# Performance work log

Hardware: AMD Instinct MI355X
Metric: run time of the kernel (lower is better)

## Reference

```python
import jax, jax.numpy as jnp
import numpy as np

TEX = 256  # texture grid resolution hardcoded in the module


def _grid_sample_bilinear(img, grid):
    """torch.F.grid_sample(img, grid): bilinear, zero padding, align_corners=False.
    img: [B,C,H,W]; grid: [B,Hg,Wg,2] in [-1,1] (x,y order). Returns [B,C,Hg,Wg]."""
    B, C, H, W = img.shape
    gx = (grid[..., 0] + 1.0) * (W * 0.5) - 0.5  # pixel-space x
    gy = (grid[..., 1] + 1.0) * (H * 0.5) - 0.5  # pixel-space y
    x0 = jnp.floor(gx)
    y0 = jnp.floor(gy)
    wx1 = gx - x0
    wy1 = gy - y0

    def corner(xi, yi, w):
        valid = (xi >= 0) & (xi <= W - 1) & (yi >= 0) & (yi <= H - 1)
        xc = jnp.clip(xi, 0, W - 1).astype(jnp.int32)
        yc = jnp.clip(yi, 0, H - 1).astype(jnp.int32)
        # per-batch gather: [B,C,Hg,Wg]
        v = jax.vmap(lambda im, yy, xx: im[:, yy, xx])(img, yc, xc)
        return v * (w * valid.astype(img.dtype))[:, None, :, :]

    return (corner(x0, y0, (1 - wx1) * (1 - wy1))
            + corner(x0 + 1, y0, wx1 * (1 - wy1))
            + corner(x0, y0 + 1, (1 - wx1) * wy1)
            + corner(x0 + 1, y0 + 1, wx1 * wy1))


def setup_inputs() -> dict:
    key = jax.random.key(0)
    k1, k2, k3, k4, k5, k6 = jax.random.split(key, 6)
    B, V, P, HW = 16, 5023, 60000, 512
    source_img = jax.random.uniform(k1, (B, 3, HW, HW), dtype=jnp.float32)
    target_mesh_v = jax.random.normal(k2, (B, V, 3), dtype=jnp.float32) * 0.1
    vertex_normals = jax.random.normal(k3, (B, V, 3), dtype=jnp.float32)
    # camera: [scale, tx, ty]; scale near 8-10 typical for DECA crops, keep ~1 range here
    camera_params = jnp.concatenate([
        jax.random.uniform(k4, (B, 1), minval=5.0, maxval=10.0),
        jax.random.uniform(k4, (B, 2), minval=-0.05, maxval=0.05)], axis=1).astype(jnp.float32)
    valid_pixel_3d_faces = jax.random.randint(k5, (P, 3), 0, V, dtype=jnp.int32)
    bc = jax.random.uniform(k6, (P, 3), dtype=jnp.float32) + 1e-3
    valid_pixel_b_coords = bc / jnp.sum(bc, axis=1, keepdims=True)  # barycentric
    lin = jnp.arange(P, dtype=jnp.int32)  # collision-free texel enumeration
    x_coords = lin % TEX
    y_coords = lin // TEX
    return {"source_img": source_img, "target_mesh_v": target_mesh_v,
            "vertex_normals": vertex_normals, "camera_params": camera_params,
            "valid_pixel_3d_faces": valid_pixel_3d_faces,
            "valid_pixel_b_coords": valid_pixel_b_coords,
            "x_coords": x_coords, "y_coords": y_coords}


def reference(source_img, target_mesh_v, vertex_normals, camera_params,
              valid_pixel_3d_faces, valid_pixel_b_coords, x_coords, y_coords):
    B = source_img.shape[0]
    # gather face vertices and barycentric-interpolate: [B,P,3(verts),3(xyz)] -> [B,P,3]
    tv = target_mesh_v[:, valid_pixel_3d_faces, :]
    pixel_3d_points = jnp.einsum('bpkc,pk->bpc', tv, valid_pixel_b_coords)
    # batch_orth_proj: scale * (xy + txy); then flip y
    cam = camera_params[:, None, :]  # [B,1,3]
    proj_xy = cam[..., 0:1] * (pixel_3d_points[..., :2] + cam[..., 1:3])
    proj_xy = jnp.stack([proj_xy[..., 0], -proj_xy[..., 1]], axis=-1)  # [B,P,2]
    # scatter into 256x256 sampling grid (zeros elsewhere)
    texture_grid = jnp.zeros((B, TEX, TEX, 2), dtype=jnp.float32)
    texture_grid = texture_grid.at[:, y_coords, x_coords, :].set(proj_xy)
    texture_img = _grid_sample_bilinear(source_img, texture_grid)  # [B,3,256,256]
    # interpolated normal z-component for visibility
    nvz = vertex_normals[..., 2][:, valid_pixel_3d_faces]  # [B,P,3]
    pixel_nz = jnp.einsum('bpk,pk->bp', nvz, valid_pixel_b_coords)
    texture_vis_mask = jnp.zeros((B, 1, TEX, TEX), dtype=jnp.bool_)
    texture_vis_mask = texture_vis_mask.at[:, 0, y_coords, x_coords].set(pixel_nz < 0)
    return texture_img, texture_vis_mask
```

## Files before the change

### kernel.cpp

```cpp
#include <hip/hip_runtime.h>
#include <math.h>

#define TEXD 256
#define NT (TEXD * TEXD)
#define BB 16
#define NPAIR (BB / 2)

struct alignas(4) F3 { float x, y, z; };
struct alignas(4) I3 { int a, b, c; };


__global__ void flame_prep_kernel(const float* __restrict__ tmv,
                                  const float* __restrict__ vn,
                                  float4* __restrict__ pv, int V,
                                  const float* __restrict__ img,
                                  uchar4* __restrict__ img8,
                                  int HW, int packBlocks) {
    int bid = blockIdx.x;
    if (bid < packBlocks) {
        int i = bid * 256 + threadIdx.x;
        if (i < BB * V) {
            int b = i / V;
            int v = i - b * V;
            pv[(size_t)v * BB + b] =
                make_float4(tmv[(size_t)i * 3 + 0], tmv[(size_t)i * 3 + 1],
                            vn[(size_t)i * 3 + 2], 0.0f);
        }
    } else {
        int plane = HW * HW;
        int cb = bid - packBlocks;
        int pb = plane / 256;
        int b = cb / pb;
        int off = (cb - b * pb) * 256 + threadIdx.x;
        const float* base = img + (size_t)b * 3 * plane;
        float r = base[off];
        float g = base[off + plane];
        float bl = base[off + 2 * plane];
        img8[(size_t)b * plane + off] =
            make_uchar4((unsigned char)__float2int_rn(r * 255.0f),
                        (unsigned char)__float2int_rn(g * 255.0f),
                        (unsigned char)__float2int_rn(bl * 255.0f), 0);
    }
}

__global__ void flame_project_kernel(const float4* __restrict__ pv,
                                     const float* __restrict__ cam,
                                     const I3* __restrict__ faces,
                                     const F3* __restrict__ bcw,
                                     float4* __restrict__ gridpair,
                                     float* __restrict__ out_mask,
                                     int P) {
    int gid = blockIdx.x * 256 + threadIdx.x;
    int t = gid >> 2;
    int q = gid & 3;

    int bs0 = 2 * q;
    int bs1 = 2 * q + 1;

    float gx[4], gy[4], mk[4];
    if (t < P) {
        I3 f3 = faces[t];
        F3 w3 = bcw[t];
        const float4* ra = pv + (size_t)f3.a * BB;
        const float4* rb = pv + (size_t)f3.b * BB;
        const float4* rc = pv + (size_t)f3.c * BB;
#pragma unroll
        for (int j = 0; j < 4; ++j) {
            int b = (j & 1) ? bs1 : bs0;
            if (j >= 2) b += NPAIR;
            float4 A = ra[b];
            float4 Bv = rb[b];
            float4 C = rc[b];
            float px = A.x * w3.x + Bv.x * w3.y + C.x * w3.z;
            float py = A.y * w3.x + Bv.y * w3.y + C.y * w3.z;
            float nz = A.z * w3.x + Bv.z * w3.y + C.z * w3.z;
            float fo = cam[b * 3 + 0];
            float cx = cam[b * 3 + 1];
            float cy = cam[b * 3 + 2];
            gx[j] = fo * (px + cx);
            gy[j] = -(fo * (py + cy));
            mk[j] = (nz < 0.0f) ? 1.0f : 0.0f;
        }
    } else {
#pragma unroll
        for (int j = 0; j < 4; ++j) { gx[j] = 0.0f; gy[j] = 0.0f; mk[j] = 0.0f; }
    }

    gridpair[(size_t)bs0 * NT + t] = make_float4(gx[0], gy[0], gx[2], gy[2]);
    gridpair[(size_t)bs1 * NT + t] = make_float4(gx[1], gy[1], gx[3], gy[3]);
    out_mask[(size_t)bs0 * NT + t] = mk[0];
    out_mask[(size_t)bs1 * NT + t] = mk[1];
    out_mask[(size_t)(bs0 + NPAIR) * NT + t] = mk[2];
    out_mask[(size_t)(bs1 + NPAIR) * NT + t] = mk[3];
}

__device__ __forceinline__ void sample3_u8(const uchar4* __restrict__ base,
                                           int HW, float gxn, float gyn,
                                           float out[3]) {
    float half = 0.5f * (float)HW;
    float gx = (gxn + 1.0f) * half - 0.5f;
    float gy = (gyn + 1.0f) * half - 0.5f;

    float x0f = floorf(gx);
    float y0f = floorf(gy);
    float wx = gx - x0f;
    float wy = gy - y0f;
    int x0 = (int)x0f;
    int y0 = (int)y0f;
    int x1 = x0 + 1;
    int y1 = y0 + 1;

    bool vx0 = (x0 >= 0) && (x0 <= HW - 1);
    bool vx1 = (x1 >= 0) && (x1 <= HW - 1);
    bool vy0 = (y0 >= 0) && (y0 <= HW - 1);
    bool vy1 = (y1 >= 0) && (y1 <= HW - 1);

    const float s = 1.0f / 255.0f;
    float w00 = (1.0f - wx) * (1.0f - wy) * ((vx0 && vy0) ? s : 0.0f);
    float w01 = wx * (1.0f - wy) * ((vx1 && vy0) ? s : 0.0f);
    float w10 = (1.0f - wx) * wy * ((vx0 && vy1) ? s : 0.0f);
    float w11 = wx * wy * ((vx1 && vy1) ? s : 0.0f);

    int xb = min(max(x0, 0), HW - 2);
    bool lo = (x0 == xb);
    float wl0 = lo ? w00 : w01;
    float wh0 = lo ? w01 : w00;
    float wl1 = lo ? w10 : w11;
    float wh1 = lo ? w11 : w10;

    int cy0 = min(max(y0, 0), HW - 1);
    int cy1 = min(max(y1, 0), HW - 1);
    const uchar4* r0 = base + (size_t)cy0 * HW + xb;
    const uchar4* r1 = base + (size_t)cy1 * HW + xb;
    uchar4 a0 = r0[0], a1 = r0[1];
    uchar4 d0 = r1[0], d1 = r1[1];

    out[0] = a0.x * wl0 + a1.x * wh0 + d0.x * wl1 + d1.x * wh1;
    out[1] = a0.y * wl0 + a1.y * wh0 + d0.y * wl1 + d1.y * wh1;
    out[2] = a0.z * wl0 + a1.z * wh0 + d0.z * wl1 + d1.z * wh1;
}

__global__ void flame_gather_kernel(const uchar4* __restrict__ img8,
                                    const float4* __restrict__ gridpair,
                                    float* __restrict__ out_img,
                                    int HW) {
    int pair = blockIdx.x % NPAIR;
    int tile = blockIdx.x / NPAIR;
    int t = tile * 256 + threadIdx.x;

    float4 g = gridpair[(size_t)pair * NT + t];
    int b0 = pair;
    int b1 = pair + NPAIR;
    size_t plane = (size_t)HW * HW;

    float o0[3], o1[3];
    sample3_u8(img8 + (size_t)b0 * plane, HW, g.x, g.y, o0);
    sample3_u8(img8 + (size_t)b1 * plane, HW, g.z, g.w, o1);

#pragma unroll
    for (int c = 0; c < 3; ++c) {
        __builtin_nontemporal_store(o0[c], out_img + ((size_t)(b0 * 3 + c)) * NT + t);
        __builtin_nontemporal_store(o1[c], out_img + ((size_t)(b1 * 3 + c)) * NT + t);
    }
}

extern "C" void kernel_launch(void* const* d_in, const int* in_sizes, int n_in,
                              void* d_out, int out_size, void* d_ws, size_t ws_size,
                              hipStream_t stream) {
    const float* source_img = (const float*)d_in[0];
    const float* tmv        = (const float*)d_in[1];
    const float* vn         = (const float*)d_in[2];
    const float* cam        = (const float*)d_in[3];
    const int*   faces      = (const int*)d_in[4];
    const float* bcw        = (const float*)d_in[5];

    int B = in_sizes[3] / 3;
    int P = in_sizes[4] / 3;
    int V = in_sizes[1] / (3 * B);
    int HW = (int)(sqrt((double)(in_sizes[0] / (3 * B))) + 0.5);

    char* wsb = (char*)d_ws;
    float4* pv = (float4*)wsb;
    wsb += (size_t)B * V * sizeof(float4);
    float4* gridpair = (float4*)wsb;
    wsb += (size_t)NPAIR * NT * sizeof(float4);
    uchar4* img8 = (uchar4*)wsb;

    float* out_img = (float*)d_out;
    float* out_mask = out_img + (size_t)B * 3 * NT;

    int packBlocks = (B * V + 255) / 256;
    int convBlocks = B * (HW * HW / 256);
    flame_prep_kernel<<<packBlocks + convBlocks, 256, 0, stream>>>(
        tmv, vn, pv, V, source_img, img8, HW, packBlocks);

    flame_project_kernel<<<4 * NT / 256, 256, 0, stream>>>(
        pv, cam, (const I3*)faces, (const F3*)bcw, gridpair, out_mask, P);

    flame_gather_kernel<<<NPAIR * (NT / 256), 256, 0, stream>>>(
        img8, gridpair, out_img, HW);
}
```

Measured before the change: 122.2 us.

## Fuse projection into gather kernel and vectorize image u8 packing

Folds the per-texel barycentric projection and mask computation into the bilinear sampling kernel, so the intermediate grid buffer no longer goes through memory and one kernel launch disappears. The packed vertex layout is permuted so that each batch pair's two entries sit next to each other and load as adjacent float4s. The image conversion now handles four pixels per thread with float4 loads and a uint4 store. In exchange, each vertex gather is now repeated across the 8 pair blocks instead of being shared by one thread group.

```diff
diff --git a/kernel.cpp b/kernel.cpp
--- a/kernel.cpp
+++ b/kernel.cpp
@@ -9,6 +9,13 @@
 struct alignas(4) F3 { float x, y, z; };
 struct alignas(4) I3 { int a, b, c; };
 
+
+__device__ __forceinline__ unsigned int packrgb(float r, float g, float b) {
+    unsigned int ri = (unsigned int)__float2int_rn(r * 255.0f);
+    unsigned int gi = (unsigned int)__float2int_rn(g * 255.0f);
+    unsigned int bi = (unsigned int)__float2int_rn(b * 255.0f);
+    return ri | (gi << 8) | (bi << 16);
+}
 
 __global__ void flame_prep_kernel(const float* __restrict__ tmv,
                                   const float* __restrict__ vn,
@@ -22,76 +29,27 @@
         if (i < BB * V) {
             int b = i / V;
             int v = i - b * V;
-            pv[(size_t)v * BB + b] =
+            pv[(size_t)v * BB + (b & 7) * 2 + (b >> 3)] =
                 make_float4(tmv[(size_t)i * 3 + 0], tmv[(size_t)i * 3 + 1],
                             vn[(size_t)i * 3 + 2], 0.0f);
         }
     } else {
         int plane = HW * HW;
         int cb = bid - packBlocks;
-        int pb = plane / 256;
-        int b = cb / pb;
-        int off = (cb - b * pb) * 256 + threadIdx.x;
+        int b = cb & 15;
+        int sub = cb >> 4;
+        int off = sub * 1024 + threadIdx.x * 4;
         const float* base = img + (size_t)b * 3 * plane;
-        float r = base[off];
-        float g = base[off + plane];
-        float bl = base[off + 2 * plane];
-        img8[(size_t)b * plane + off] =
-            make_uchar4((unsigned char)__float2int_rn(r * 255.0f),
-                        (unsigned char)__float2int_rn(g * 255.0f),
-                        (unsigned char)__float2int_rn(bl * 255.0f), 0);
+        float4 r  = *(const float4*)(base + off);
+        float4 g  = *(const float4*)(base + plane + off);
+        float4 bl = *(const float4*)(base + 2 * plane + off);
+        uint4 st;
+        st.x = packrgb(r.x, g.x, bl.x);
+        st.y = packrgb(r.y, g.y, bl.y);
+        st.z = packrgb(r.z, g.z, bl.z);
+        st.w = packrgb(r.w, g.w, bl.w);
+        *reinterpret_cast<uint4*>(img8 + (size_t)b * plane + off) = st;
     }
-}
-
-__global__ void flame_project_kernel(const float4* __restrict__ pv,
-                                     const float* __restrict__ cam,
-                                     const I3* __restrict__ faces,
-                                     const F3* __restrict__ bcw,
-                                     float4* __restrict__ gridpair,
-                                     float* __restrict__ out_mask,
-                                     int P) {
-    int gid = blockIdx.x * 256 + threadIdx.x;
-    int t = gid >> 2;
-    int q = gid & 3;
-
-    int bs0 = 2 * q;
-    int bs1 = 2 * q + 1;
-
-    float gx[4], gy[4], mk[4];
-    if (t < P) {
-        I3 f3 = faces[t];
-        F3 w3 = bcw[t];
-        const float4* ra = pv + (size_t)f3.a * BB;
-        const float4* rb = pv + (size_t)f3.b * BB;
-        const float4* rc = pv + (size_t)f3.c * BB;
-#pragma unroll
-        for (int j = 0; j < 4; ++j) {
-            int b = (j & 1) ? bs1 : bs0;
-            if (j >= 2) b += NPAIR;
-            float4 A = ra[b];
-            float4 Bv = rb[b];
-            float4 C = rc[b];
-            float px = A.x * w3.x + Bv.x * w3.y + C.x * w3.z;
-            float py = A.y * w3.x + Bv.y * w3.y + C.y * w3.z;
-            float nz = A.z * w3.x + Bv.z * w3.y + C.z * w3.z;
-            float fo = cam[b * 3 + 0];
-            float cx = cam[b * 3 + 1];
-            float cy = cam[b * 3 + 2];
-            gx[j] = fo * (px + cx);
-            gy[j] = -(fo * (py + cy));
-            mk[j] = (nz < 0.0f) ? 1.0f : 0.0f;
-        }
-    } else {
-#pragma unroll
-        for (int j = 0; j < 4; ++j) { gx[j] = 0.0f; gy[j] = 0.0f; mk[j] = 0.0f; }
-    }
-
-    gridpair[(size_t)bs0 * NT + t] = make_float4(gx[0], gy[0], gx[2], gy[2]);
-    gridpair[(size_t)bs1 * NT + t] = make_float4(gx[1], gy[1], gx[3], gy[3]);
-    out_mask[(size_t)bs0 * NT + t] = mk[0];
-    out_mask[(size_t)bs1 * NT + t] = mk[1];
-    out_mask[(size_t)(bs0 + NPAIR) * NT + t] = mk[2];
-    out_mask[(size_t)(bs1 + NPAIR) * NT + t] = mk[3];
 }
 
 __device__ __forceinline__ void sample3_u8(const uchar4* __restrict__ base,
@@ -140,28 +98,61 @@
     out[2] = a0.z * wl0 + a1.z * wh0 + d0.z * wl1 + d1.z * wh1;
 }
 
-__global__ void flame_gather_kernel(const uchar4* __restrict__ img8,
-                                    const float4* __restrict__ gridpair,
-                                    float* __restrict__ out_img,
-                                    int HW) {
-    int pair = blockIdx.x % NPAIR;
-    int tile = blockIdx.x / NPAIR;
-    int t = tile * 256 + threadIdx.x;
-
-    float4 g = gridpair[(size_t)pair * NT + t];
+__global__ void flame_fused_kernel(const float4* __restrict__ pv,
+                                   const float* __restrict__ cam,
+                                   const I3* __restrict__ faces,
+                                   const F3* __restrict__ bcw,
+                                   const uchar4* __restrict__ img8,
+                                   float* __restrict__ out_img,
+                                   float* __restrict__ out_mask,
+                                   int P, int HW) {
+    int pair = blockIdx.x & (NPAIR - 1);
+    int t = (blockIdx.x >> 3) * 256 + threadIdx.x;
     int b0 = pair;
     int b1 = pair + NPAIR;
+
+    float gx0 = 0.0f, gy0 = 0.0f, gx1 = 0.0f, gy1 = 0.0f;
+    float mk0 = 0.0f, mk1 = 0.0f;
+    if (t < P) {
+        I3 f3 = faces[t];
+        F3 w3 = bcw[t];
+        const float4* ra = pv + (size_t)f3.a * BB + pair * 2;
+        const float4* rb = pv + (size_t)f3.b * BB + pair * 2;
+        const float4* rc = pv + (size_t)f3.c * BB + pair * 2;
+        float4 A0 = ra[0], A1 = ra[1];
+        float4 B0 = rb[0], B1 = rb[1];
+        float4 C0 = rc[0], C1 = rc[1];
+
+        float f0 = cam[b0 * 3 + 0], cx0 = cam[b0 * 3 + 1], cy0 = cam[b0 * 3 + 2];
+        float f1 = cam[b1 * 3 + 0], cx1 = cam[b1 * 3 + 1], cy1 = cam[b1 * 3 + 2];
+
+        float px0 = A0.x * w3.x + B0.x * w3.y + C0.x * w3.z;
+        float py0 = A0.y * w3.x + B0.y * w3.y + C0.y * w3.z;
+        float nz0 = A0.z * w3.x + B0.z * w3.y + C0.z * w3.z;
+        float px1 = A1.x * w3.x + B1.x * w3.y + C1.x * w3.z;
+        float py1 = A1.y * w3.x + B1.y * w3.y + C1.y * w3.z;
+        float nz1 = A1.z * w3.x + B1.z * w3.y + C1.z * w3.z;
+
+        gx0 = f0 * (px0 + cx0);
+        gy0 = -(f0 * (py0 + cy0));
+        mk0 = (nz0 < 0.0f) ? 1.0f : 0.0f;
+        gx1 = f1 * (px1 + cx1);
+        gy1 = -(f1 * (py1 + cy1));
+        mk1 = (nz1 < 0.0f) ? 1.0f : 0.0f;
+    }
+
     size_t plane = (size_t)HW * HW;
-
     float o0[3], o1[3];
-    sample3_u8(img8 + (size_t)b0 * plane, HW, g.x, g.y, o0);
-    sample3_u8(img8 + (size_t)b1 * plane, HW, g.z, g.w, o1);
+    sample3_u8(img8 + (size_t)b0 * plane, HW, gx0, gy0, o0);
+    sample3_u8(img8 + (size_t)b1 * plane, HW, gx1, gy1, o1);
 
 #pragma unroll
     for (int c = 0; c < 3; ++c) {
         __builtin_nontemporal_store(o0[c], out_img + ((size_t)(b0 * 3 + c)) * NT + t);
         __builtin_nontemporal_store(o1[c], out_img + ((size_t)(b1 * 3 + c)) * NT + t);
     }
+    __builtin_nontemporal_store(mk0, out_mask + (size_t)b0 * NT + t);
+    __builtin_nontemporal_store(mk1, out_mask + (size_t)b1 * NT + t);
 }
 
 extern "C" void kernel_launch(void* const* d_in, const int* in_sizes, int n_in,
@@ -182,21 +173,16 @@
     char* wsb = (char*)d_ws;
     float4* pv = (float4*)wsb;
     wsb += (size_t)B * V * sizeof(float4);
-    float4* gridpair = (float4*)wsb;
-    wsb += (size_t)NPAIR * NT * sizeof(float4);
     uchar4* img8 = (uchar4*)wsb;
 
     float* out_img = (float*)d_out;
     float* out_mask = out_img + (size_t)B * 3 * NT;
 
-    int packBlocks = (B * V + 255) / 256;
-    int convBlocks = B * (HW * HW / 256);
+    int packBlocks = (((B * V + 255) / 256) + 7) & ~7;
+    int convBlocks = B * (HW * HW / 1024);
     flame_prep_kernel<<<packBlocks + convBlocks, 256, 0, stream>>>(
         tmv, vn, pv, V, source_img, img8, HW, packBlocks);
 
-    flame_project_kernel<<<4 * NT / 256, 256, 0, stream>>>(
-        pv, cam, (const I3*)faces, (const F3*)bcw, gridpair, out_mask, P);
-
-    flame_gather_kernel<<<NPAIR * (NT / 256), 256, 0, stream>>>(
-        img8, gridpair, out_img, HW);
+    flame_fused_kernel<<<NPAIR * (NT / 256), 256, 0, stream>>>(
+        pv, cam, (const I3*)faces, (const F3*)bcw, img8, out_img, out_mask, P, HW);
 }
```

Result: slower. 124.7 us (+2.1%).
